# Kernel optimization log

Measured on AMD Instinct MI355X. Metric: run time of the kernel, lower is better.

Reference implementation:

```python
import jax, jax.numpy as jnp
import numpy as np

DELTA = 1e-7
INDEX = (0, 1)  # hops to process, matches init index=[0,1]


def _divide_no_nan(num, den):
    # tf.math.divide_no_nan semantics: 0 where denominator is 0
    safe = jnp.where(den == 0, 1.0, den)
    return jnp.where(den == 0, 0.0, num / safe)


def setup_inputs() -> dict:
    key = jax.random.key(0)
    k1, k2, k3, k4 = jax.random.split(key, 4)
    B, N, F1 = 8, 2048, 4          # F1 = 1 population + 3 SIR features
    T, C = 2, 64                   # hops available, output channels
    input_feature = jax.random.uniform(k1, (B, N, F1), dtype=jnp.float32)
    OD_all = jax.random.uniform(k2, (B, T, N, N), dtype=jnp.float32)
    kernel = jax.random.normal(k3, (3 * 2 ** len(INDEX), C), dtype=jnp.float32)
    bias = jax.random.normal(k4, (C,), dtype=jnp.float32)
    return {"input_feature": input_feature, "OD_all": OD_all,
            "kernel": kernel, "bias": bias}


def reference(input_feature, OD_all, kernel, bias):
    populations = input_feature[:, :, :1]   # [B,N,1]
    SIR = input_feature[:, :, 1:]           # [B,N,F]
    for idx in INDEX:
        OD = OD_all[:, idx]                                  # [B,N,N]
        SIR_n = _divide_no_nan(SIR, DELTA + populations)     # [B,N,F]
        row_sum = jnp.sum(OD, axis=2, keepdims=True)         # [B,N,1]
        ratio = _divide_no_nan(populations, DELTA + row_sum)  # [B,N,1]
        OD = jnp.where(ratio < 1, OD * ratio, OD)            # clip outflow
        OD_out = jnp.sum(OD, axis=2, keepdims=True)          # [B,N,1]
        OD_in = jnp.sum(OD, axis=1)                          # [B,N]
        SIR_in = jnp.einsum('bij,bif->bjf', OD, SIR_n)       # OD^T @ SIR_n
        SIR_stay = SIR - OD_out * SIR_n
        populations = populations - OD_out + OD_in[..., None]
        SIR = jnp.concatenate([SIR_stay, SIR_in], axis=-1)   # doubles F
    output = jnp.einsum('bnf,fc->bnc', SIR, kernel) + bias
    output = jax.nn.relu(output)
    return jnp.concatenate([populations, output], axis=-1)   # [B,N,1+C]
```

## Files before the change

kernel.cpp:

```cpp
#include <hip/hip_runtime.h>


#define DELTA 1e-7f
constexpr int B = 8, N = 2048, T = 2;
constexpr int NB = B * N;

constexpr int RS_OFF   = 0;
constexpr int W0_OFF   = RS_OFF  + 2 * NB;
constexpr int ST0_OFF  = W0_OFF  + NB * 4;
constexpr int W1_OFF   = ST0_OFF + NB * 4;
constexpr int ST1_OFF  = W1_OFF  + NB * 8;
constexpr int ACC0_OFF = ST1_OFF + NB * 8;
constexpr int ACC1_OFF = ACC0_OFF + NB * 4;
constexpr int WS_END   = ACC1_OFF + NB * 7;

__global__ void __launch_bounds__(256) rowsum_kernel(const float* __restrict__ OD,
                                                     float* __restrict__ rs) {
  const int quad = threadIdx.x >> 6, lane = threadIdx.x & 63;
  const int r = blockIdx.x * 4 + quad;
  const float4* p = (const float4*)(OD + (size_t)r * N);
  float s = 0.f;
#pragma unroll
  for (int k = 0; k < 8; ++k) {
    float4 v = p[lane + 64 * k];
    s += (v.x + v.y) + (v.z + v.w);
  }
#pragma unroll
  for (int off = 32; off; off >>= 1) s += __shfl_down(s, off, 64);
  if (lane == 0) {
    const int b = r >> 12, t = (r >> 11) & 1, i = r & (N - 1);
    rs[t * NB + b * N + i] = s;
  }
}

__global__ void __launch_bounds__(256) prep0_kernel(const float* __restrict__ feat,
                                                    const float* __restrict__ rs,
                                                    float* __restrict__ w0,
                                                    float* __restrict__ st0) {
  const int g = blockIdx.x * 256 + threadIdx.x;
  const float4 f = ((const float4*)feat)[g];
  const float pop = f.x;
  const float rs0 = rs[g];
  const float ratio = pop / (DELTA + rs0);
  const float scale = ratio < 1.f ? ratio : 1.f;
  const float inv = 1.f / (DELTA + pop);
  const float sn0 = f.y * inv, sn1 = f.z * inv, sn2 = f.w * inv;
  const float odout = scale * rs0;
  ((float4*)w0)[g]  = make_float4(scale, scale * sn0, scale * sn1, scale * sn2);
  ((float4*)st0)[g] = make_float4(pop - odout, f.y - odout * sn0,
                                  f.z - odout * sn1, f.w - odout * sn2);
}

template <int NF, int WSTRIDE>
__global__ void __launch_bounds__(256) colacc_kernel(const float* __restrict__ OD_all,
                                                     const int t,
                                                     const float* __restrict__ w,
                                                     float* __restrict__ acc) {
  const int tid = threadIdx.x;
  const int quad = tid >> 6, lane = tid & 63;
  const int jbase = blockIdx.x * 256;
  const int ibase = blockIdx.y * 256;
  const int b = blockIdx.z;

  __shared__ float wlds[256 * WSTRIDE];
  {
    const float4* src = (const float4*)(w + (size_t)(b * N + ibase) * WSTRIDE);
    float4* dst = (float4*)wlds;
#pragma unroll
    for (int x = tid; x < 256 * WSTRIDE / 4; x += 256) dst[x] = src[x];
  }
  __syncthreads();

  float accr[4][NF];
#pragma unroll
  for (int c = 0; c < 4; ++c)
#pragma unroll
    for (int f = 0; f < NF; ++f) accr[c][f] = 0.f;

  const float* odbase =
      OD_all + ((size_t)(b * T + t) * N + ibase) * N + jbase + lane * 4;
  for (int k = 0; k < 64; ++k) {
    const int r = quad + 4 * k;
    const float4 od = *(const float4*)(odbase + (size_t)r * N);
#pragma unroll
    for (int f = 0; f < NF; ++f) {
      const float wv = wlds[r * WSTRIDE + f];
      accr[0][f] += od.x * wv;
      accr[1][f] += od.y * wv;
      accr[2][f] += od.z * wv;
      accr[3][f] += od.w * wv;
    }
  }
  __syncthreads();

  __shared__ float red[4][256 * NF];
#pragma unroll
  for (int c = 0; c < 4; ++c)
#pragma unroll
    for (int f = 0; f < NF; ++f)
      red[quad][(lane * 4 + c) * NF + f] = accr[c][f];
  __syncthreads();

  for (int x = tid; x < 256 * NF; x += 256) {
    const float s = red[0][x] + red[1][x] + red[2][x] + red[3][x];
    const int colx = x / NF, f = x - colx * NF;
    atomicAdd(&acc[(size_t)(b * N + jbase + colx) * NF + f], s);
  }
}

__global__ void __launch_bounds__(256) prep1_kernel(const float* __restrict__ st0,
                                                    const float* __restrict__ acc0,
                                                    const float* __restrict__ rs,
                                                    float* __restrict__ w1,
                                                    float* __restrict__ st1) {
  const int g = blockIdx.x * 256 + threadIdx.x;
  const float4 s0 = ((const float4*)st0)[g];
  const float4 a0 = ((const float4*)acc0)[g];
  const float rs1 = rs[NB + g];
  const float pop = s0.x + a0.x;
  const float S[6] = {s0.y, s0.z, s0.w, a0.y, a0.z, a0.w};
  const float ratio = pop / (DELTA + rs1);
  const float scale = ratio < 1.f ? ratio : 1.f;
  const float inv = 1.f / (DELTA + pop);
  const float odout = scale * rs1;
  float wv[8], sv[8];
  wv[0] = scale;
  sv[0] = pop - odout;
#pragma unroll
  for (int f = 0; f < 6; ++f) {
    const float sn = S[f] * inv;
    wv[1 + f] = scale * sn;
    sv[1 + f] = S[f] - odout * sn;
  }
  wv[7] = 0.f;
  sv[7] = 0.f;
  float4* w4 = (float4*)(w1 + (size_t)g * 8);
  w4[0] = make_float4(wv[0], wv[1], wv[2], wv[3]);
  w4[1] = make_float4(wv[4], wv[5], wv[6], wv[7]);
  float4* s4 = (float4*)(st1 + (size_t)g * 8);
  s4[0] = make_float4(sv[0], sv[1], sv[2], sv[3]);
  s4[1] = make_float4(sv[4], sv[5], sv[6], sv[7]);
}

__global__ void __launch_bounds__(256) final_kernel(const float* __restrict__ st1,
                                                    const float* __restrict__ acc1,
                                                    const float* __restrict__ kern,
                                                    const float* __restrict__ bias,
                                                    float* __restrict__ out) {
  __shared__ float klds[12 * 64];
  const int tid = threadIdx.x;
  if (tid < 192) ((float4*)klds)[tid] = ((const float4*)kern)[tid];
  __syncthreads();
  const int p = blockIdx.x * 4 + (tid >> 6);
  const int c = tid & 63;
  const float4* s4 = (const float4*)(st1 + (size_t)p * 8);
  const float4 l0 = s4[0], l1 = s4[1];
  const float* a = acc1 + (size_t)p * 7;
  const float S[12] = {l0.y, l0.z, l0.w, l1.x, l1.y, l1.z,
                       a[1], a[2], a[3], a[4], a[5], a[6]};
  float sum = bias[c];
#pragma unroll
  for (int f = 0; f < 12; ++f) sum += S[f] * klds[f * 64 + c];
  float* o = out + (size_t)p * 65;
  o[1 + c] = sum > 0.f ? sum : 0.f;
  if (c == 0) o[0] = l0.x + a[0];
}

extern "C" void kernel_launch(void* const* d_in, const int* in_sizes, int n_in,
                              void* d_out, int out_size, void* d_ws, size_t ws_size,
                              hipStream_t stream) {
  const float* feat = (const float*)d_in[0];
  const float* OD   = (const float*)d_in[1];
  const float* kern = (const float*)d_in[2];
  const float* bias = (const float*)d_in[3];
  float* out = (float*)d_out;
  float* ws = (float*)d_ws;

  float* rs   = ws + RS_OFF;
  float* w0   = ws + W0_OFF;
  float* st0  = ws + ST0_OFF;
  float* w1   = ws + W1_OFF;
  float* st1  = ws + ST1_OFF;
  float* acc0 = ws + ACC0_OFF;
  float* acc1 = ws + ACC1_OFF;

  hipMemsetAsync(acc0, 0, (size_t)(WS_END - ACC0_OFF) * sizeof(float), stream);

  rowsum_kernel<<<2 * NB / 4, 256, 0, stream>>>(OD, rs);
  prep0_kernel<<<NB / 256, 256, 0, stream>>>(feat, rs, w0, st0);
  dim3 gc(N / 256, N / 256, B);
  colacc_kernel<4, 4><<<gc, 256, 0, stream>>>(OD, 0, w0, acc0);
  prep1_kernel<<<NB / 256, 256, 0, stream>>>(st0, acc0, rs, w1, st1);
  colacc_kernel<7, 8><<<gc, 256, 0, stream>>>(OD, 1, w1, acc1);
  final_kernel<<<NB / 4, 256, 0, stream>>>(st1, acc1, kern, bias, out);
}
```

Measured before the change: 416.9 us.

## Split rowsum per hop for cache reuse, halve colacc row tile, prefetch OD rows

The row-sum pass is split into two launches, one per hop. The hop-1 row sum now runs right before its use, so the hop-1 OD slice may still be in the large last-level cache when colacc reads it. The colacc row tile shrinks from 256 to 128, doubling the grid for more parallelism at the cost of twice as many atomic reductions. A one-row software prefetch is added so each OD load overlaps the FMAs of the previous row, which adds some register pressure.

```diff
diff --git a/kernel.cpp b/kernel.cpp
--- a/kernel.cpp
+++ b/kernel.cpp
@@ -14,11 +14,13 @@
 constexpr int ACC1_OFF = ACC0_OFF + NB * 4;
 constexpr int WS_END   = ACC1_OFF + NB * 7;
 
-__global__ void __launch_bounds__(256) rowsum_kernel(const float* __restrict__ OD,
+__global__ void __launch_bounds__(256) rowsum_kernel(const float* __restrict__ OD_all,
+                                                     const int t,
                                                      float* __restrict__ rs) {
   const int quad = threadIdx.x >> 6, lane = threadIdx.x & 63;
   const int r = blockIdx.x * 4 + quad;
-  const float4* p = (const float4*)(OD + (size_t)r * N);
+  const int b = r >> 11, i = r & (N - 1);
+  const float4* p = (const float4*)(OD_all + ((size_t)(b * T + t) * N + i) * N);
   float s = 0.f;
 #pragma unroll
   for (int k = 0; k < 8; ++k) {
@@ -27,10 +29,7 @@
   }
 #pragma unroll
   for (int off = 32; off; off >>= 1) s += __shfl_down(s, off, 64);
-  if (lane == 0) {
-    const int b = r >> 12, t = (r >> 11) & 1, i = r & (N - 1);
-    rs[t * NB + b * N + i] = s;
-  }
+  if (lane == 0) rs[t * NB + r] = s;
 }
 
 __global__ void __launch_bounds__(256) prep0_kernel(const float* __restrict__ feat,
@@ -56,18 +55,20 @@
                                                      const int t,
                                                      const float* __restrict__ w,
                                                      float* __restrict__ acc) {
+  constexpr int TI = 128;
+  constexpr int KI = TI / 4;
   const int tid = threadIdx.x;
   const int quad = tid >> 6, lane = tid & 63;
   const int jbase = blockIdx.x * 256;
-  const int ibase = blockIdx.y * 256;
+  const int ibase = blockIdx.y * TI;
   const int b = blockIdx.z;
 
-  __shared__ float wlds[256 * WSTRIDE];
+  __shared__ float wlds[TI * WSTRIDE];
   {
     const float4* src = (const float4*)(w + (size_t)(b * N + ibase) * WSTRIDE);
     float4* dst = (float4*)wlds;
 #pragma unroll
-    for (int x = tid; x < 256 * WSTRIDE / 4; x += 256) dst[x] = src[x];
+    for (int x = tid; x < TI * WSTRIDE / 4; x += 256) dst[x] = src[x];
   }
   __syncthreads();
 
@@ -79,17 +80,20 @@
 
   const float* odbase =
       OD_all + ((size_t)(b * T + t) * N + ibase) * N + jbase + lane * 4;
-  for (int k = 0; k < 64; ++k) {
+  float4 cur = *(const float4*)(odbase + (size_t)quad * N);
+  for (int k = 0; k < KI; ++k) {
     const int r = quad + 4 * k;
-    const float4 od = *(const float4*)(odbase + (size_t)r * N);
+    float4 nxt;
+    if (k + 1 < KI) nxt = *(const float4*)(odbase + (size_t)(r + 4) * N);
 #pragma unroll
     for (int f = 0; f < NF; ++f) {
       const float wv = wlds[r * WSTRIDE + f];
-      accr[0][f] += od.x * wv;
-      accr[1][f] += od.y * wv;
-      accr[2][f] += od.z * wv;
-      accr[3][f] += od.w * wv;
+      accr[0][f] += cur.x * wv;
+      accr[1][f] += cur.y * wv;
+      accr[2][f] += cur.z * wv;
+      accr[3][f] += cur.w * wv;
     }
+    cur = nxt;
   }
   __syncthreads();
 
@@ -186,10 +190,11 @@
 
   hipMemsetAsync(acc0, 0, (size_t)(WS_END - ACC0_OFF) * sizeof(float), stream);
 
-  rowsum_kernel<<<2 * NB / 4, 256, 0, stream>>>(OD, rs);
+  dim3 gc(N / 256, N / 128, B);
+  rowsum_kernel<<<NB / 4, 256, 0, stream>>>(OD, 0, rs);
   prep0_kernel<<<NB / 256, 256, 0, stream>>>(feat, rs, w0, st0);
-  dim3 gc(N / 256, N / 256, B);
   colacc_kernel<4, 4><<<gc, 256, 0, stream>>>(OD, 0, w0, acc0);
+  rowsum_kernel<<<NB / 4, 256, 0, stream>>>(OD, 1, rs);
   prep1_kernel<<<NB / 256, 256, 0, stream>>>(st0, acc0, rs, w1, st1);
   colacc_kernel<7, 8><<<gc, 256, 0, stream>>>(OD, 1, w1, acc1);
   final_kernel<<<NB / 4, 256, 0, stream>>>(st1, acc1, kern, bias, out);
```

New measurement: 418.7 us. Within noise of the previous version (+0.4%).

## Fuse row-sum with column accumulation so OD is read once per hop

Applied to the files above, without the earlier changes.

Row sums, outflow scaling and the OD^T·w accumulation now happen in a single pass. Each block of 512 threads owns 64 full rows and software-prefetches them, so the separate rowsum pass that re-read all of OD is gone. The atomic column accumulation is replaced by per-row-block partial buffers, which a separate reduction kernel sums, and the memset is removed. In exchange, only 256 blocks are launched and there are per-8-row block syncs plus extra partial-sum traffic.

```diff
diff --git a/kernel.cpp b/kernel.cpp
--- a/kernel.cpp
+++ b/kernel.cpp
@@ -2,144 +2,208 @@
 
 
 #define DELTA 1e-7f
-constexpr int B = 8, N = 2048, T = 2;
+constexpr int B = 8, N = 2048;
 constexpr int NB = B * N;
-
-constexpr int RS_OFF   = 0;
-constexpr int W0_OFF   = RS_OFF  + 2 * NB;
-constexpr int ST0_OFF  = W0_OFF  + NB * 4;
-constexpr int W1_OFF   = ST0_OFF + NB * 4;
-constexpr int ST1_OFF  = W1_OFF  + NB * 8;
-constexpr int ACC0_OFF = ST1_OFF + NB * 8;
-constexpr int ACC1_OFF = ACC0_OFF + NB * 4;
-constexpr int WS_END   = ACC1_OFF + NB * 7;
-
-__global__ void __launch_bounds__(256) rowsum_kernel(const float* __restrict__ OD,
-                                                     float* __restrict__ rs) {
-  const int quad = threadIdx.x >> 6, lane = threadIdx.x & 63;
-  const int r = blockIdx.x * 4 + quad;
-  const float4* p = (const float4*)(OD + (size_t)r * N);
-  float s = 0.f;
-#pragma unroll
-  for (int k = 0; k < 8; ++k) {
-    float4 v = p[lane + 64 * k];
-    s += (v.x + v.y) + (v.z + v.w);
-  }
-#pragma unroll
-  for (int off = 32; off; off >>= 1) s += __shfl_down(s, off, 64);
-  if (lane == 0) {
-    const int b = r >> 12, t = (r >> 11) & 1, i = r & (N - 1);
-    rs[t * NB + b * N + i] = s;
-  }
-}
-
-__global__ void __launch_bounds__(256) prep0_kernel(const float* __restrict__ feat,
-                                                    const float* __restrict__ rs,
-                                                    float* __restrict__ w0,
-                                                    float* __restrict__ st0) {
+constexpr int RPB = 64;
+constexpr int NRB = N / RPB;
+
+constexpr int ST0_OFF  = 0;
+constexpr int PRE_OFF  = ST0_OFF + NB * 4;
+constexpr int ST1_OFF  = PRE_OFF + NB * 8;
+constexpr int P0_OFF   = ST1_OFF + NB * 8;
+constexpr int P1_OFF   = P0_OFF + B * NRB * N * 4;
+constexpr int ACC1_OFF = P1_OFF + B * NRB * N * 8;
+
+__device__ __forceinline__ void fma4(float4& a, float s, const float4& w) {
+  a.x = fmaf(s, w.x, a.x);
+  a.y = fmaf(s, w.y, a.y);
+  a.z = fmaf(s, w.z, a.z);
+  a.w = fmaf(s, w.w, a.w);
+}
+
+__global__ void __launch_bounds__(512) fused0_kernel(const float* __restrict__ OD,
+                                                     const float* __restrict__ feat,
+                                                     float* __restrict__ part0,
+                                                     float* __restrict__ st0) {
+  const int tid = threadIdx.x, w = tid >> 6, l = tid & 63;
+  const int b = blockIdx.x >> 5, rb = blockIdx.x & 31, i0 = rb * RPB;
+  __shared__ float4 ldsfeat[RPB];
+  __shared__ float wpart[64];
+  __shared__ float4 wv[8];
+  if (tid < RPB) ldsfeat[tid] = ((const float4*)feat)[b * N + i0 + tid];
+  __syncthreads();
+
+  const float* odbase = OD + ((size_t)(b * 2) * N + i0) * N + w * 256 + l * 4;
+  float4 acc[4] = {};
+  float4 cur[8], nxt[8];
+#pragma unroll
+  for (int m = 0; m < 8; ++m) cur[m] = *(const float4*)(odbase + (size_t)m * N);
+
+  for (int g = 0; g < 8; ++g) {
+    if (g < 7) {
+#pragma unroll
+      for (int m = 0; m < 8; ++m)
+        nxt[m] = *(const float4*)(odbase + (size_t)((g + 1) * 8 + m) * N);
+    }
+#pragma unroll
+    for (int m = 0; m < 8; ++m) {
+      float s = (cur[m].x + cur[m].y) + (cur[m].z + cur[m].w);
+#pragma unroll
+      for (int off = 32; off; off >>= 1) s += __shfl_down(s, off, 64);
+      if (l == 0) wpart[w * 8 + m] = s;
+    }
+    __syncthreads();
+    if (tid < 8) {
+      const int r = g * 8 + tid;
+      float rs = 0.f;
+#pragma unroll
+      for (int ww = 0; ww < 8; ++ww) rs += wpart[ww * 8 + tid];
+      const float4 f = ldsfeat[r];
+      const float pop = f.x;
+      const float ratio = pop / (DELTA + rs);
+      const float scale = ratio < 1.f ? ratio : 1.f;
+      const float inv = 1.f / (DELTA + pop);
+      const float odout = scale * rs;
+      const float k1 = 1.f - odout * inv;
+      ((float4*)st0)[b * N + i0 + r] =
+          make_float4(pop - odout, f.y * k1, f.z * k1, f.w * k1);
+      wv[tid] = make_float4(scale, scale * f.y * inv, scale * f.z * inv,
+                            scale * f.w * inv);
+    }
+    __syncthreads();
+#pragma unroll
+    for (int m = 0; m < 8; ++m) {
+      const float4 wvm = wv[m];
+      fma4(acc[0], cur[m].x, wvm);
+      fma4(acc[1], cur[m].y, wvm);
+      fma4(acc[2], cur[m].z, wvm);
+      fma4(acc[3], cur[m].w, wvm);
+    }
+    if (g < 7) {
+#pragma unroll
+      for (int m = 0; m < 8; ++m) cur[m] = nxt[m];
+    }
+  }
+  float4* pb = (float4*)part0 + (size_t)blockIdx.x * N + (w * 256 + l * 4);
+#pragma unroll
+  for (int c = 0; c < 4; ++c) pb[c] = acc[c];
+}
+
+__global__ void __launch_bounds__(256) prep1_kernel(const float* __restrict__ st0,
+                                                    const float* __restrict__ part0,
+                                                    float* __restrict__ pre1) {
   const int g = blockIdx.x * 256 + threadIdx.x;
-  const float4 f = ((const float4*)feat)[g];
-  const float pop = f.x;
-  const float rs0 = rs[g];
-  const float ratio = pop / (DELTA + rs0);
-  const float scale = ratio < 1.f ? ratio : 1.f;
+  const int b = g >> 11, i = g & (N - 1);
+  float4 in = {0.f, 0.f, 0.f, 0.f};
+  const float4* p = (const float4*)part0 + (size_t)b * NRB * N + i;
+#pragma unroll 8
+  for (int rb = 0; rb < NRB; ++rb) {
+    const float4 v = p[(size_t)rb * N];
+    in.x += v.x; in.y += v.y; in.z += v.z; in.w += v.w;
+  }
+  const float4 s0 = ((const float4*)st0)[g];
+  const float pop = s0.x + in.x;
   const float inv = 1.f / (DELTA + pop);
-  const float sn0 = f.y * inv, sn1 = f.z * inv, sn2 = f.w * inv;
-  const float odout = scale * rs0;
-  ((float4*)w0)[g]  = make_float4(scale, scale * sn0, scale * sn1, scale * sn2);
-  ((float4*)st0)[g] = make_float4(pop - odout, f.y - odout * sn0,
-                                  f.z - odout * sn1, f.w - odout * sn2);
-}
-
-template <int NF, int WSTRIDE>
-__global__ void __launch_bounds__(256) colacc_kernel(const float* __restrict__ OD_all,
-                                                     const int t,
-                                                     const float* __restrict__ w,
-                                                     float* __restrict__ acc) {
-  const int tid = threadIdx.x;
-  const int quad = tid >> 6, lane = tid & 63;
-  const int jbase = blockIdx.x * 256;
-  const int ibase = blockIdx.y * 256;
-  const int b = blockIdx.z;
-
-  __shared__ float wlds[256 * WSTRIDE];
-  {
-    const float4* src = (const float4*)(w + (size_t)(b * N + ibase) * WSTRIDE);
-    float4* dst = (float4*)wlds;
-#pragma unroll
-    for (int x = tid; x < 256 * WSTRIDE / 4; x += 256) dst[x] = src[x];
-  }
+  float4* o = (float4*)pre1 + (size_t)g * 2;
+  o[0] = make_float4(pop, inv, s0.y, s0.z);
+  o[1] = make_float4(s0.w, in.y, in.z, in.w);
+}
+
+__global__ void __launch_bounds__(512) fused1_kernel(const float* __restrict__ OD,
+                                                     const float* __restrict__ pre1,
+                                                     float* __restrict__ part1,
+                                                     float* __restrict__ st1) {
+  const int tid = threadIdx.x, w = tid >> 6, l = tid & 63;
+  const int b = blockIdx.x >> 5, rb = blockIdx.x & 31, i0 = rb * RPB;
+  __shared__ float ldspre[RPB * 8];
+  __shared__ float wpart[64];
+  __shared__ float4 wva[8], wvb[8];
+  if (tid < 128)
+    ((float4*)ldspre)[tid] =
+        ((const float4*)(pre1 + (size_t)(b * N + i0) * 8))[tid];
   __syncthreads();
 
-  float accr[4][NF];
-#pragma unroll
-  for (int c = 0; c < 4; ++c)
-#pragma unroll
-    for (int f = 0; f < NF; ++f) accr[c][f] = 0.f;
-
-  const float* odbase =
-      OD_all + ((size_t)(b * T + t) * N + ibase) * N + jbase + lane * 4;
-  for (int k = 0; k < 64; ++k) {
-    const int r = quad + 4 * k;
-    const float4 od = *(const float4*)(odbase + (size_t)r * N);
-#pragma unroll
-    for (int f = 0; f < NF; ++f) {
-      const float wv = wlds[r * WSTRIDE + f];
-      accr[0][f] += od.x * wv;
-      accr[1][f] += od.y * wv;
-      accr[2][f] += od.z * wv;
-      accr[3][f] += od.w * wv;
-    }
-  }
-  __syncthreads();
-
-  __shared__ float red[4][256 * NF];
-#pragma unroll
-  for (int c = 0; c < 4; ++c)
-#pragma unroll
-    for (int f = 0; f < NF; ++f)
-      red[quad][(lane * 4 + c) * NF + f] = accr[c][f];
-  __syncthreads();
-
-  for (int x = tid; x < 256 * NF; x += 256) {
-    const float s = red[0][x] + red[1][x] + red[2][x] + red[3][x];
-    const int colx = x / NF, f = x - colx * NF;
-    atomicAdd(&acc[(size_t)(b * N + jbase + colx) * NF + f], s);
-  }
-}
-
-__global__ void __launch_bounds__(256) prep1_kernel(const float* __restrict__ st0,
-                                                    const float* __restrict__ acc0,
-                                                    const float* __restrict__ rs,
-                                                    float* __restrict__ w1,
-                                                    float* __restrict__ st1) {
+  const float* odbase = OD + ((size_t)(b * 2 + 1) * N + i0) * N + w * 256 + l * 4;
+  float4 accA[4] = {}, accB[4] = {};
+  float4 cur[8], nxt[8];
+#pragma unroll
+  for (int m = 0; m < 8; ++m) cur[m] = *(const float4*)(odbase + (size_t)m * N);
+
+  for (int g = 0; g < 8; ++g) {
+    if (g < 7) {
+#pragma unroll
+      for (int m = 0; m < 8; ++m)
+        nxt[m] = *(const float4*)(odbase + (size_t)((g + 1) * 8 + m) * N);
+    }
+#pragma unroll
+    for (int m = 0; m < 8; ++m) {
+      float s = (cur[m].x + cur[m].y) + (cur[m].z + cur[m].w);
+#pragma unroll
+      for (int off = 32; off; off >>= 1) s += __shfl_down(s, off, 64);
+      if (l == 0) wpart[w * 8 + m] = s;
+    }
+    __syncthreads();
+    if (tid < 8) {
+      const int r = g * 8 + tid;
+      float rs = 0.f;
+#pragma unroll
+      for (int ww = 0; ww < 8; ++ww) rs += wpart[ww * 8 + tid];
+      const float* pr = &ldspre[r * 8];
+      const float pop = pr[0], inv = pr[1];
+      const float ratio = pop / (DELTA + rs);
+      const float scale = ratio < 1.f ? ratio : 1.f;
+      const float odout = scale * rs;
+      const float k1 = 1.f - odout * inv;
+      float4* s4 = (float4*)st1 + (size_t)(b * N + i0 + r) * 2;
+      s4[0] = make_float4(pop - odout, pr[2] * k1, pr[3] * k1, pr[4] * k1);
+      s4[1] = make_float4(pr[5] * k1, pr[6] * k1, pr[7] * k1, 0.f);
+      const float si = scale * inv;
+      wva[tid] = make_float4(scale, pr[2] * si, pr[3] * si, pr[4] * si);
+      wvb[tid] = make_float4(pr[5] * si, pr[6] * si, pr[7] * si, 0.f);
+    }
+    __syncthreads();
+#pragma unroll
+    for (int m = 0; m < 8; ++m) {
+      const float4 wa = wva[m], wb = wvb[m];
+      fma4(accA[0], cur[m].x, wa);
+      fma4(accB[0], cur[m].x, wb);
+      fma4(accA[1], cur[m].y, wa);
+      fma4(accB[1], cur[m].y, wb);
+      fma4(accA[2], cur[m].z, wa);
+      fma4(accB[2], cur[m].z, wb);
+      fma4(accA[3], cur[m].w, wa);
+      fma4(accB[3], cur[m].w, wb);
+    }
+    if (g < 7) {
+#pragma unroll
+      for (int m = 0; m < 8; ++m) cur[m] = nxt[m];
+    }
+  }
+  float4* pb =
+      (float4*)part1 + ((size_t)blockIdx.x * N + (w * 256 + l * 4)) * 2;
+#pragma unroll
+  for (int c = 0; c < 4; ++c) {
+    pb[c * 2] = accA[c];
+    pb[c * 2 + 1] = accB[c];
+  }
+}
+
+__global__ void __launch_bounds__(256) reduce1_kernel(const float* __restrict__ part1,
+                                                      float* __restrict__ acc1) {
   const int g = blockIdx.x * 256 + threadIdx.x;
-  const float4 s0 = ((const float4*)st0)[g];
-  const float4 a0 = ((const float4*)acc0)[g];
-  const float rs1 = rs[NB + g];
-  const float pop = s0.x + a0.x;
-  const float S[6] = {s0.y, s0.z, s0.w, a0.y, a0.z, a0.w};
-  const float ratio = pop / (DELTA + rs1);
-  const float scale = ratio < 1.f ? ratio : 1.f;
-  const float inv = 1.f / (DELTA + pop);
-  const float odout = scale * rs1;
-  float wv[8], sv[8];
-  wv[0] = scale;
-  sv[0] = pop - odout;
-#pragma unroll
-  for (int f = 0; f < 6; ++f) {
-    const float sn = S[f] * inv;
-    wv[1 + f] = scale * sn;
-    sv[1 + f] = S[f] - odout * sn;
-  }
-  wv[7] = 0.f;
-  sv[7] = 0.f;
-  float4* w4 = (float4*)(w1 + (size_t)g * 8);
-  w4[0] = make_float4(wv[0], wv[1], wv[2], wv[3]);
-  w4[1] = make_float4(wv[4], wv[5], wv[6], wv[7]);
-  float4* s4 = (float4*)(st1 + (size_t)g * 8);
-  s4[0] = make_float4(sv[0], sv[1], sv[2], sv[3]);
-  s4[1] = make_float4(sv[4], sv[5], sv[6], sv[7]);
+  const int b = g >> 11, j = g & (N - 1);
+  float4 a = {0.f, 0.f, 0.f, 0.f}, c = {0.f, 0.f, 0.f, 0.f};
+  const float4* p = (const float4*)part1 + ((size_t)b * NRB * N + j) * 2;
+#pragma unroll 8
+  for (int rb = 0; rb < NRB; ++rb) {
+    const float4 va = p[(size_t)rb * N * 2];
+    const float4 vb = p[(size_t)rb * N * 2 + 1];
+    a.x += va.x; a.y += va.y; a.z += va.z; a.w += va.w;
+    c.x += vb.x; c.y += vb.y; c.z += vb.z; c.w += vb.w;
+  }
+  float4* o = (float4*)acc1 + (size_t)g * 2;
+  o[0] = a;
+  o[1] = c;
 }
 
 __global__ void __launch_bounds__(256) final_kernel(const float* __restrict__ st1,
@@ -153,17 +217,18 @@
   __syncthreads();
   const int p = blockIdx.x * 4 + (tid >> 6);
   const int c = tid & 63;
-  const float4* s4 = (const float4*)(st1 + (size_t)p * 8);
+  const float4* s4 = (const float4*)st1 + (size_t)p * 2;
   const float4 l0 = s4[0], l1 = s4[1];
-  const float* a = acc1 + (size_t)p * 7;
+  const float4* a4 = (const float4*)acc1 + (size_t)p * 2;
+  const float4 a0 = a4[0], a1 = a4[1];
   const float S[12] = {l0.y, l0.z, l0.w, l1.x, l1.y, l1.z,
-                       a[1], a[2], a[3], a[4], a[5], a[6]};
+                       a0.y, a0.z, a0.w, a1.x, a1.y, a1.z};
   float sum = bias[c];
 #pragma unroll
   for (int f = 0; f < 12; ++f) sum += S[f] * klds[f * 64 + c];
   float* o = out + (size_t)p * 65;
   o[1 + c] = sum > 0.f ? sum : 0.f;
-  if (c == 0) o[0] = l0.x + a[0];
+  if (c == 0) o[0] = l0.x + a0.x;
 }
 
 extern "C" void kernel_launch(void* const* d_in, const int* in_sizes, int n_in,
@@ -176,21 +241,16 @@
   float* out = (float*)d_out;
   float* ws = (float*)d_ws;
 
-  float* rs   = ws + RS_OFF;
-  float* w0   = ws + W0_OFF;
-  float* st0  = ws + ST0_OFF;
-  float* w1   = ws + W1_OFF;
-  float* st1  = ws + ST1_OFF;
-  float* acc0 = ws + ACC0_OFF;
-  float* acc1 = ws + ACC1_OFF;
-
-  hipMemsetAsync(acc0, 0, (size_t)(WS_END - ACC0_OFF) * sizeof(float), stream);
-
-  rowsum_kernel<<<2 * NB / 4, 256, 0, stream>>>(OD, rs);
-  prep0_kernel<<<NB / 256, 256, 0, stream>>>(feat, rs, w0, st0);
-  dim3 gc(N / 256, N / 256, B);
-  colacc_kernel<4, 4><<<gc, 256, 0, stream>>>(OD, 0, w0, acc0);
-  prep1_kernel<<<NB / 256, 256, 0, stream>>>(st0, acc0, rs, w1, st1);
-  colacc_kernel<7, 8><<<gc, 256, 0, stream>>>(OD, 1, w1, acc1);
+  float* st0   = ws + ST0_OFF;
+  float* pre1  = ws + PRE_OFF;
+  float* st1   = ws + ST1_OFF;
+  float* part0 = ws + P0_OFF;
+  float* part1 = ws + P1_OFF;
+  float* acc1  = ws + ACC1_OFF;
+
+  fused0_kernel<<<B * NRB, 512, 0, stream>>>(OD, feat, part0, st0);
+  prep1_kernel<<<NB / 256, 256, 0, stream>>>(st0, part0, pre1);
+  fused1_kernel<<<B * NRB, 512, 0, stream>>>(OD, pre1, part1, st1);
+  reduce1_kernel<<<NB / 256, 256, 0, stream>>>(part1, acc1);
   final_kernel<<<NB / 4, 256, 0, stream>>>(st1, acc1, kern, bias, out);
 }
```

After: 401.7 us. 1.04x faster.
